# Optimization experiments

Measured on AMD Instinct MI355X. Metric: run time of the kernel, lower is better.

The kernel has to match this reference:

```python
import jax, jax.numpy as jnp
import numpy as np

B, C, T, V, P = 32, 64, 512, 54, 4
EPS = 1e-5


def setup_inputs() -> dict:
    key = jax.random.key(0)
    ks = jax.random.split(key, 5)
    x = jax.random.normal(ks[0], (B, C, T, V), dtype=jnp.float32)
    A = jax.random.uniform(ks[1], (P, V, V), dtype=jnp.float32)
    gweights = jax.random.normal(ks[2], (P, V, V), dtype=jnp.float32)
    W = jax.random.normal(ks[3], (P, C, C), dtype=jnp.float32) * 0.05  # (P, C_out, C_in)
    b = jax.random.normal(ks[4], (P, C), dtype=jnp.float32) * 0.05
    gamma = jnp.ones((C,), dtype=jnp.float32)
    beta = jnp.zeros((C,), dtype=jnp.float32)
    return {"x": x, "A": A, "gweights": gweights, "W": W, "b": b,
            "gamma": gamma, "beta": beta}


def reference(x, A, gweights, W, b, gamma, beta):
    # x: (B, C_in, T, V)
    Aeff = A * gweights  # (P, V, V), learned-weighted adjacency
    # per-part graph aggregation (x @ A_p) followed by 1x1 conv, summed over parts
    # out[b,o,t,v] = sum_p sum_c sum_u x[b,c,t,u] * Aeff[p,u,v] * W[p,o,c] + sum_p b[p,o]
    y = jnp.einsum('bctu,puv,poc->botv', x, Aeff, W, optimize=True)
    y = y + jnp.sum(b, axis=0)[None, :, None, None]
    # BatchNorm2d in training mode: batch stats over (B, T, V) per channel
    mean = jnp.mean(y, axis=(0, 2, 3), keepdims=True)
    var = jnp.mean(jnp.square(y - mean), axis=(0, 2, 3), keepdims=True)
    y = (y - mean) * jax.lax.rsqrt(var + EPS)
    y = y * gamma[None, :, None, None] + beta[None, :, None, None]
    y = jax.nn.relu(y)
    # temporal_conv is Identity (kernel_size=None); residual shortcut is Identity (C_in==C_out)
    return y + x
```

## Files before the change

### kernel.cpp

```cpp
#include <hip/hip_runtime.h>
#include <hip/hip_bf16.h>


typedef __bf16 bf16_t;
typedef __bf16 bf16x8 __attribute__((ext_vector_type(8)));
typedef __bf16 bf16x4 __attribute__((ext_vector_type(4)));
typedef float  f32x4  __attribute__((ext_vector_type(4)));
typedef unsigned int uint32;

static __device__ __forceinline__ f32x4 mfma16(bf16x8 a, bf16x8 b, f32x4 c) {
  return __builtin_amdgcn_mfma_f32_16x16x32_bf16(a, b, c, 0, 0, 0);
}
static __device__ __forceinline__ uint32 pk2(float a, float b) {
  union { __bf16 h; unsigned short u; } ua, ub;
  ua.h = (__bf16)a; ub.h = (__bf16)b;
  return (uint32)ua.u | ((uint32)ub.u << 16);
}

__global__ __launch_bounds__(256) void k_prep(
    const float* __restrict__ A, const float* __restrict__ g,
    const float* __restrict__ W, const float* __restrict__ bias,
    bf16_t* __restrict__ Wstk, bf16_t* __restrict__ At,
    float* __restrict__ bsum, float* __restrict__ stats) {
  int i = blockIdx.x * 256 + threadIdx.x;
  if (i < 16384) Wstk[i] = (bf16_t)W[i];
  if (i < 64 * 224) {
    int v = i / 224, pu = i - v * 224;
    float val = 0.f;
    if (v < 54 && pu < 216) { int idx = pu * 54 + v; val = A[idx] * g[idx]; }
    At[i] = (bf16_t)val;
  }
  if (i < 64) {
    float s = 0.f;
    for (int p = 0; p < 4; ++p) s += bias[p * 64 + i];
    bsum[i] = s;
  }
  if (i < 8192) stats[i] = 0.f;
}

__global__ __launch_bounds__(256) void k_tr(const float* __restrict__ x,
                                            bf16_t* __restrict__ xT) {
  __shared__ bf16_t T[256 * 66];
  const int tid = threadIdx.x;
  const int b = blockIdx.x / 108;
  const int rblk = blockIdx.x - b * 108;
  const int r0 = rblk << 8;
  const float* xb = x + (size_t)b * 64 * 27648 + r0;
  #pragma unroll 4
  for (int j = 0; j < 16; ++j) {
    int idx = tid + (j << 8);
    int c = idx >> 6, r4 = idx & 63;
    const float* src = xb + (size_t)c * 27648 + r4;
    #pragma unroll
    for (int k = 0; k < 4; ++k) {
      float v = src[k << 6];
      T[(r4 + (k << 6)) * 66 + c] = (bf16_t)v;
    }
  }
  __syncthreads();
  bf16_t* outb = xT + (((size_t)b * 27648 + r0) << 6);
  const uint32* Td = (const uint32*)T;
  #pragma unroll
  for (int j = 0; j < 8; ++j) {
    int row = (tid >> 3) + (j << 5);
    int seg = tid & 7;
    uint32 d0 = Td[row * 33 + (seg << 2) + 0];
    uint32 d1 = Td[row * 33 + (seg << 2) + 1];
    uint32 d2 = Td[row * 33 + (seg << 2) + 2];
    uint32 d3 = Td[row * 33 + (seg << 2) + 3];
    uint4 vv = make_uint4(d0, d1, d2, d3);
    *(uint4*)(outb + ((size_t)row << 6) + (seg << 3)) = vv;
  }
}

#define UPS 232

template<bool YBF16>
__global__ __launch_bounds__(256) void k_pass1(
    const bf16_t* __restrict__ xT, const bf16_t* __restrict__ Wstk,
    const bf16_t* __restrict__ At, const float* __restrict__ bsum,
    void* __restrict__ yprev, float* __restrict__ stats) {
  __shared__ bf16_t UpS[2][64 * UPS];

  const int tid  = threadIdx.x;
  const int bid  = blockIdx.x;
  const int b    = bid >> 7;
  const int t0   = (bid & 127) << 2;
  const int w    = tid >> 6;
  const int L    = tid & 63;
  const int quad = L >> 4;
  const int l15  = L & 15;

  for (int i = tid; i < 1024; i += 256) {
    int buf = i >> 9, row = (i >> 3) & 63, d = i & 7;
    ((uint32*)UpS[buf])[row * 116 + 108 + d] = 0u;
  }

  bf16x8 wb[4][2];
  #pragma unroll
  for (int ot = 0; ot < 4; ++ot)
    #pragma unroll
    for (int kk = 0; kk < 2; ++kk)
      wb[ot][kk] = *(const bf16x8*)(Wstk + (((w << 6) + (ot << 4) + l15) << 6)
                                          + (kk << 5) + (quad << 3));

  const int oc = (w << 4) + l15;
  const float bsv = bsum[oc];
  float ssum = 0.f, ssq = 0.f;

  for (int tt = 0; tt < 4; ++tt) {
    bf16_t* Up = UpS[tt & 1];
    const int t = t0 + tt;

    const bf16_t* xbase = xT + (((size_t)b * 27648 + (size_t)t * 54) << 6);
    bf16x8 xa[4][2];
    #pragma unroll
    for (int ut = 0; ut < 4; ++ut)
      #pragma unroll
      for (int kk = 0; kk < 2; ++kk)
        xa[ut][kk] = *(const bf16x8*)(xbase + (((ut << 4) + l15) << 6)
                                            + (kk << 5) + (quad << 3));
    #pragma unroll
    for (int ut = 0; ut < 4; ++ut) {
      const int u0 = (ut << 4) + (quad << 2);
      #pragma unroll
      for (int ot = 0; ot < 4; ++ot) {
        f32x4 acc = {0.f, 0.f, 0.f, 0.f};
        acc = mfma16(xa[ut][0], wb[ot][0], acc);
        acc = mfma16(xa[ut][1], wb[ot][1], acc);
        if (u0 < 54) {
          uint32* dst = (uint32*)(Up + ((ot << 4) + l15) * UPS + w * 54 + u0);
          dst[0] = pk2(acc[0], acc[1]);
          if (u0 + 3 < 54) dst[1] = pk2(acc[2], acc[3]);
        }
      }
    }
    __syncthreads();

    bf16x8 ub[7];
    #pragma unroll
    for (int kk = 0; kk < 7; ++kk)
      ub[kk] = *(const bf16x8*)(Up + ((w << 4) + l15) * UPS + (kk << 5) + (quad << 3));

    const size_t obase = (((size_t)((b << 6) + oc) << 9) + (size_t)t) * 54;
    #pragma unroll
    for (int mi = 0; mi < 4; ++mi) {
      f32x4 acc = {0.f, 0.f, 0.f, 0.f};
      #pragma unroll
      for (int kk = 0; kk < 7; ++kk) {
        bf16x8 av = *(const bf16x8*)(At + ((mi << 4) + l15) * 224
                                        + (kk << 5) + (quad << 3));
        acc = mfma16(av, ub[kk], acc);
      }
      const int v0 = (mi << 4) + (quad << 2);
      if (v0 + 3 < 54) {
        float y0 = acc[0] + bsv, y1 = acc[1] + bsv, y2 = acc[2] + bsv, y3 = acc[3] + bsv;
        if (YBF16) {
          uint32* d = (uint32*)((bf16_t*)yprev + obase + v0);
          d[0] = pk2(y0, y1); d[1] = pk2(y2, y3);
        } else {
          float2* d = (float2*)((float*)yprev + obase + v0);
          d[0] = make_float2(y0, y1); d[1] = make_float2(y2, y3);
        }
        ssum += y0 + y1 + y2 + y3;
        ssq  += y0 * y0 + y1 * y1 + y2 * y2 + y3 * y3;
      } else if (v0 == 52) {
        float y0 = acc[0] + bsv, y1 = acc[1] + bsv;
        if (YBF16) {
          *(uint32*)((bf16_t*)yprev + obase + v0) = pk2(y0, y1);
        } else {
          *(float2*)((float*)yprev + obase + v0) = make_float2(y0, y1);
        }
        ssum += y0 + y1;
        ssq  += y0 * y0 + y1 * y1;
      }
    }
    __syncthreads();
  }

  ssum += __shfl_xor(ssum, 16); ssq += __shfl_xor(ssq, 16);
  ssum += __shfl_xor(ssum, 32); ssq += __shfl_xor(ssq, 32);
  if (L < 16) {
    float* sb = stats + (bid & 63) * 128;
    atomicAdd(&sb[oc], ssum);
    atomicAdd(&sb[64 + oc], ssq);
  }
}

#define XT_STRIDE 72
#define UP_STRIDE 232
__global__ __launch_bounds__(256) void k_pass1_legacy(
    const float* __restrict__ x, const bf16_t* __restrict__ Wstk,
    const bf16_t* __restrict__ At, const float* __restrict__ bsum,
    float* __restrict__ ypre, float* __restrict__ stats) {
  __shared__ bf16_t XtS[4 * 54 * XT_STRIDE];
  __shared__ bf16_t UpS[64 * UP_STRIDE];
  const int tid = threadIdx.x, bid = blockIdx.x;
  const int b = bid >> 7, t0 = (bid & 127) << 2;
  const int w = tid >> 6, L = tid & 63, quad = L >> 4, l15 = L & 15;
  for (int i = tid; i < 64 * 8; i += 256)
    UpS[(i >> 3) * UP_STRIDE + 216 + (i & 7)] = (bf16_t)0.0f;
  const float* xb = x + (size_t)(b * 64 * 512 + t0) * 54;
  for (int j = tid; j < 64 * 216; j += 256) {
    int c = j / 216, r = j - c * 216;
    float v = xb[(size_t)c * 27648 + r];
    int tt = r / 54, u = r - tt * 54;
    XtS[(tt * 54 + u) * XT_STRIDE + c] = (bf16_t)v;
  }
  bf16x8 wfr[4][2];
  #pragma unroll
  for (int mi = 0; mi < 4; ++mi) {
    const bf16_t* arow = Wstk + (((((w << 2) + mi) << 4) + l15) * 64) + (quad << 3);
    #pragma unroll
    for (int kk = 0; kk < 2; ++kk) wfr[mi][kk] = *(const bf16x8*)(arow + kk * 32);
  }
  const int obase = (w << 4) + (quad << 2);
  float bs[4];
  #pragma unroll
  for (int r = 0; r < 4; ++r) bs[r] = bsum[obase + r];
  bf16x8 zf;
  #pragma unroll
  for (int j = 0; j < 8; ++j) zf[j] = (bf16_t)0.0f;
  float ssum[4] = {0.f,0.f,0.f,0.f}, ssq[4] = {0.f,0.f,0.f,0.f};
  __syncthreads();
  for (int tt = 0; tt < 4; ++tt) {
    bf16x8 xfr[4][2];
    #pragma unroll
    for (int nt = 0; nt < 4; ++nt) {
      const int urow = (nt << 4) + l15;
      #pragma unroll
      for (int kk = 0; kk < 2; ++kk) {
        xfr[nt][kk] = zf;
        if (urow < 54)
          xfr[nt][kk] = *(const bf16x8*)(&XtS[(tt * 54 + urow) * XT_STRIDE + kk * 32 + (quad << 3)]);
      }
    }
    #pragma unroll
    for (int mi = 0; mi < 4; ++mi) {
      f32x4 acc[4];
      #pragma unroll
      for (int nt = 0; nt < 4; ++nt)
        #pragma unroll
        for (int e = 0; e < 4; ++e) acc[nt][e] = 0.f;
      #pragma unroll
      for (int kk = 0; kk < 2; ++kk)
        #pragma unroll
        for (int nt = 0; nt < 4; ++nt)
          acc[nt] = mfma16(wfr[mi][kk], xfr[nt][kk], acc[nt]);
      #pragma unroll
      for (int nt = 0; nt < 4; ++nt) {
        const int u = (nt << 4) + l15;
        if (u < 54)
          #pragma unroll
          for (int r = 0; r < 4; ++r) {
            int o = (mi << 4) + (quad << 2) + r;
            UpS[o * UP_STRIDE + w * 54 + u] = (bf16_t)acc[nt][r];
          }
      }
    }
    __syncthreads();
    bf16x8 afr[7];
    #pragma unroll
    for (int kk = 0; kk < 7; ++kk)
      afr[kk] = *(const bf16x8*)(&UpS[((w << 4) + l15) * UP_STRIDE + kk * 32 + (quad << 3)]);
    f32x4 acc[4];
    #pragma unroll
    for (int nt = 0; nt < 4; ++nt)
      #pragma unroll
      for (int e = 0; e < 4; ++e) acc[nt][e] = 0.f;
    #pragma unroll
    for (int kk = 0; kk < 7; ++kk)
      #pragma unroll
      for (int nt = 0; nt < 4; ++nt) {
        bf16x8 bfr = *(const bf16x8*)(At + ((nt << 4) + l15) * 224 + kk * 32 + (quad << 3));
        acc[nt] = mfma16(afr[kk], bfr, acc[nt]);
      }
    const int t = t0 + tt;
    #pragma unroll
    for (int nt = 0; nt < 4; ++nt) {
      const int vcol = (nt << 4) + l15;
      if (vcol < 54)
        #pragma unroll
        for (int r = 0; r < 4; ++r) {
          float yv = acc[nt][r] + bs[r];
          ypre[(((size_t)b * 64 + (obase + r)) * 512 + t) * 54 + vcol] = yv;
          ssum[r] += yv; ssq[r] += yv * yv;
        }
    }
    __syncthreads();
  }
  #pragma unroll
  for (int off = 1; off < 16; off <<= 1)
    #pragma unroll
    for (int r = 0; r < 4; ++r) {
      ssum[r] += __shfl_xor(ssum[r], off);
      ssq[r]  += __shfl_xor(ssq[r], off);
    }
  if (l15 == 0) {
    float* sb = stats + (bid & 63) * 128;
    #pragma unroll
    for (int r = 0; r < 4; ++r) {
      atomicAdd(&sb[obase + r], ssum[r]);
      atomicAdd(&sb[64 + obase + r], ssq[r]);
    }
  }
}

__global__ void k_finalize(const float* __restrict__ gamma, const float* __restrict__ beta,
                           const float* __restrict__ stats, float* __restrict__ ac) {
  int o = threadIdx.x;
  if (o >= 64) return;
  float S = 0.f, Q = 0.f;
  for (int buf = 0; buf < 64; ++buf) {
    S += stats[buf * 128 + o];
    Q += stats[buf * 128 + 64 + o];
  }
  const float inv = 1.0f / 884736.0f;
  float mean = S * inv;
  float var  = Q * inv - mean * mean;
  float a = gamma[o] * rsqrtf(var + 1e-5f);
  ac[o] = a;
  ac[64 + o] = beta[o] - mean * a;
}

template<bool YBF16>
__global__ __launch_bounds__(256) void k_pass2(const float* __restrict__ x,
                                               const float* __restrict__ ac,
                                               const void* __restrict__ yprev,
                                               float* __restrict__ out) {
  const int slab = blockIdx.y;
  const int o = slab & 63;
  const size_t base = (size_t)slab * 27648 + (size_t)(((blockIdx.x << 8) + threadIdx.x) << 2);
  const float a = ac[o], c = ac[64 + o];
  float y0, y1, y2, y3;
  if (YBF16) {
    bf16x4 yp = *(const bf16x4*)((const bf16_t*)yprev + base);
    y0 = (float)yp[0]; y1 = (float)yp[1]; y2 = (float)yp[2]; y3 = (float)yp[3];
  } else {
    float4 yp = *(const float4*)((const float*)yprev + base);
    y0 = yp.x; y1 = yp.y; y2 = yp.z; y3 = yp.w;
  }
  float4 xv = *(const float4*)(x + base);
  float4 r;
  r.x = fmaxf(fmaf(a, y0, c), 0.f) + xv.x;
  r.y = fmaxf(fmaf(a, y1, c), 0.f) + xv.y;
  r.z = fmaxf(fmaf(a, y2, c), 0.f) + xv.z;
  r.w = fmaxf(fmaf(a, y3, c), 0.f) + xv.w;
  *(float4*)(out + base) = r;
}

extern "C" void kernel_launch(void* const* d_in, const int* in_sizes, int n_in,
                              void* d_out, int out_size, void* d_ws, size_t ws_size,
                              hipStream_t stream) {
  const float* x     = (const float*)d_in[0];
  const float* A     = (const float*)d_in[1];
  const float* g     = (const float*)d_in[2];
  const float* W     = (const float*)d_in[3];
  const float* bias  = (const float*)d_in[4];
  const float* gamma = (const float*)d_in[5];
  const float* beta  = (const float*)d_in[6];

  char* ws = (char*)d_ws;
  bf16_t* Wstk  = (bf16_t*)(ws + 0);
  bf16_t* At    = (bf16_t*)(ws + 32768);
  float*  bsum  = (float*)(ws + 61440);
  float*  stats = (float*)(ws + 61696);
  float*  ac    = (float*)(ws + 94464);
  const size_t XT_OFF   = 98304;
  const size_t XT_BYTES = (size_t)32 * 27648 * 64 * 2;
  const size_t YP_OFF   = XT_OFF + XT_BYTES;
  bf16_t* xT = (bf16_t*)(ws + XT_OFF);
  float*  out = (float*)d_out;

  const size_t need_primary = YP_OFF + XT_BYTES + 4096;
  const size_t need_fbA     = YP_OFF + 4096;

  k_prep<<<64, 256, 0, stream>>>(A, g, W, bias, Wstk, At, bsum, stats);

  if (ws_size >= need_primary) {
    bf16_t* ypre = (bf16_t*)(ws + YP_OFF);
    k_tr<<<3456, 256, 0, stream>>>(x, xT);
    k_pass1<true><<<4096, 256, 0, stream>>>(xT, Wstk, At, bsum, ypre, stats);
    k_finalize<<<1, 64, 0, stream>>>(gamma, beta, stats, ac);
    k_pass2<true><<<dim3(27, 2048), 256, 0, stream>>>(x, ac, ypre, out);
  } else if (ws_size >= need_fbA) {
    k_tr<<<3456, 256, 0, stream>>>(x, xT);
    k_pass1<false><<<4096, 256, 0, stream>>>(xT, Wstk, At, bsum, out, stats);
    k_finalize<<<1, 64, 0, stream>>>(gamma, beta, stats, ac);
    k_pass2<false><<<dim3(27, 2048), 256, 0, stream>>>(x, ac, out, out);
  } else {
    k_pass1_legacy<<<4096, 256, 0, stream>>>(x, Wstk, At, bsum, out, stats);
    k_finalize<<<1, 64, 0, stream>>>(gamma, beta, stats, ac);
    k_pass2<false><<<dim3(27, 2048), 256, 0, stream>>>(x, ac, out, out);
  }
}
```

Baseline: 610.5 us.

## Reorder einsum to apply adjacency first and drop transpose pass

Removes the separate x transpose kernel and its bf16 workspace copy. pass1 now reads fp32 x directly along the contiguous (t,v) axis, converts it to bf16 in registers, and multiplies by the adjacency first to form Z[v,(p,c)] in shared memory. A second MFMA stage contracts Z against a stacked W over K=256. It also prefetches the next timestep's x, uses a single shared buffer, and adds a launch-bounds occupancy hint. The first-stage loads are strided per lane, with a clamp to avoid reading past the end of x, and the contraction over u now includes padding work.

Measured after the change: 768.3 us. +25.8%, slower.

```diff
diff --git a/kernel.cpp b/kernel.cpp
--- a/kernel.cpp
+++ b/kernel.cpp
@@ -16,19 +16,52 @@
   ua.h = (__bf16)a; ub.h = (__bf16)b;
   return (uint32)ua.u | ((uint32)ub.u << 16);
 }
+static __device__ __forceinline__ bf16x8 cvt8(float2 a, float2 b, float2 c, float2 d) {
+  union { uint32 u[4]; bf16x8 v; } r;
+  r.u[0] = pk2(a.x, a.y); r.u[1] = pk2(b.x, b.y);
+  r.u[2] = pk2(c.x, c.y); r.u[3] = pk2(d.x, d.y);
+  return r.v;
+}
+
+#define XTOT 56623104ull
+
+static __device__ __forceinline__ void loadx(float2* pf, const float* __restrict__ x,
+                                             size_t xr) {
+  pf[0] = *(const float2*)(x + xr);
+  pf[1] = *(const float2*)(x + xr + 2);
+  pf[2] = *(const float2*)(x + xr + 4);
+  pf[3] = *(const float2*)(x + xr + 6);
+  const size_t LIM = XTOT - 2;
+  size_t o0 = xr + 32, o1 = xr + 34, o2 = xr + 36, o3 = xr + 38;
+  if (o0 > LIM) o0 = LIM;
+  if (o1 > LIM) o1 = LIM;
+  if (o2 > LIM) o2 = LIM;
+  if (o3 > LIM) o3 = LIM;
+  pf[4] = *(const float2*)(x + o0);
+  pf[5] = *(const float2*)(x + o1);
+  pf[6] = *(const float2*)(x + o2);
+  pf[7] = *(const float2*)(x + o3);
+}
 
 __global__ __launch_bounds__(256) void k_prep(
     const float* __restrict__ A, const float* __restrict__ g,
     const float* __restrict__ W, const float* __restrict__ bias,
-    bf16_t* __restrict__ Wstk, bf16_t* __restrict__ At,
+    bf16_t* __restrict__ W2, bf16_t* __restrict__ Ae,
     float* __restrict__ bsum, float* __restrict__ stats) {
   int i = blockIdx.x * 256 + threadIdx.x;
-  if (i < 16384) Wstk[i] = (bf16_t)W[i];
-  if (i < 64 * 224) {
-    int v = i / 224, pu = i - v * 224;
+  if (i < 16384) {
+    int o = i >> 8, k = i & 255, p = k >> 6, c = k & 63;
+    W2[i] = (bf16_t)W[p * 4096 + o * 64 + c];
+  }
+  if (i < 224 * 64) {
+    int pv = i >> 6, u = i & 63;
+    int p = pv / 56, v = pv - p * 56;
     float val = 0.f;
-    if (v < 54 && pu < 216) { int idx = pu * 54 + v; val = A[idx] * g[idx]; }
-    At[i] = (bf16_t)val;
+    if (v < 54 && u < 54) {
+      int idx = (p * 54 + u) * 54 + v;
+      val = A[idx] * g[idx];
+    }
+    Ae[i] = (bf16_t)val;
   }
   if (i < 64) {
     float s = 0.f;
@@ -38,49 +71,14 @@
   if (i < 8192) stats[i] = 0.f;
 }
 
-__global__ __launch_bounds__(256) void k_tr(const float* __restrict__ x,
-                                            bf16_t* __restrict__ xT) {
-  __shared__ bf16_t T[256 * 66];
-  const int tid = threadIdx.x;
-  const int b = blockIdx.x / 108;
-  const int rblk = blockIdx.x - b * 108;
-  const int r0 = rblk << 8;
-  const float* xb = x + (size_t)b * 64 * 27648 + r0;
-  #pragma unroll 4
-  for (int j = 0; j < 16; ++j) {
-    int idx = tid + (j << 8);
-    int c = idx >> 6, r4 = idx & 63;
-    const float* src = xb + (size_t)c * 27648 + r4;
-    #pragma unroll
-    for (int k = 0; k < 4; ++k) {
-      float v = src[k << 6];
-      T[(r4 + (k << 6)) * 66 + c] = (bf16_t)v;
-    }
-  }
-  __syncthreads();
-  bf16_t* outb = xT + (((size_t)b * 27648 + r0) << 6);
-  const uint32* Td = (const uint32*)T;
-  #pragma unroll
-  for (int j = 0; j < 8; ++j) {
-    int row = (tid >> 3) + (j << 5);
-    int seg = tid & 7;
-    uint32 d0 = Td[row * 33 + (seg << 2) + 0];
-    uint32 d1 = Td[row * 33 + (seg << 2) + 1];
-    uint32 d2 = Td[row * 33 + (seg << 2) + 2];
-    uint32 d3 = Td[row * 33 + (seg << 2) + 3];
-    uint4 vv = make_uint4(d0, d1, d2, d3);
-    *(uint4*)(outb + ((size_t)row << 6) + (seg << 3)) = vv;
-  }
-}
-
-#define UPS 232
+#define ZS 264
 
 template<bool YBF16>
-__global__ __launch_bounds__(256) void k_pass1(
-    const bf16_t* __restrict__ xT, const bf16_t* __restrict__ Wstk,
-    const bf16_t* __restrict__ At, const float* __restrict__ bsum,
+__global__ __launch_bounds__(256, 4) void k_pass1(
+    const float* __restrict__ x, const bf16_t* __restrict__ W2,
+    const bf16_t* __restrict__ Ae, const float* __restrict__ bsum,
     void* __restrict__ yprev, float* __restrict__ stats) {
-  __shared__ bf16_t UpS[2][64 * UPS];
+  __shared__ bf16_t Zt[64 * ZS];
 
   const int tid  = threadIdx.x;
   const int bid  = blockIdx.x;
@@ -91,66 +89,64 @@
   const int quad = L >> 4;
   const int l15  = L & 15;
 
-  for (int i = tid; i < 1024; i += 256) {
-    int buf = i >> 9, row = (i >> 3) & 63, d = i & 7;
-    ((uint32*)UpS[buf])[row * 116 + 108 + d] = 0u;
-  }
-
-  bf16x8 wb[4][2];
+  for (int i = tid; i < 8 * ZS / 2; i += 256)
+    ((uint32*)(Zt + 56 * ZS))[i] = 0u;
+
+  bf16x8 wf[8];
   #pragma unroll
-  for (int ot = 0; ot < 4; ++ot)
-    #pragma unroll
-    for (int kk = 0; kk < 2; ++kk)
-      wb[ot][kk] = *(const bf16x8*)(Wstk + (((w << 6) + (ot << 4) + l15) << 6)
-                                          + (kk << 5) + (quad << 3));
-
-  const int oc = (w << 4) + l15;
+  for (int kk = 0; kk < 8; ++kk)
+    wf[kk] = *(const bf16x8*)(W2 + (((w << 4) + l15) << 8) + (kk << 5) + (quad << 3));
+
+  int zoff[14];
+  #pragma unroll
+  for (int n = 0; n < 14; ++n) {
+    int pv = (n << 4) + l15;
+    int p = pv / 56;
+    int v = pv - p * 56;
+    zoff[n] = v * ZS + (p << 6) + (w << 4) + (quad << 2);
+  }
+
+  const int oc  = (w << 4) + l15;
   const float bsv = bsum[oc];
   float ssum = 0.f, ssq = 0.f;
 
+  const size_t xrow0 = (size_t)((b << 6) + oc) * 27648 + (quad << 3);
+
+  float2 pf[8];
+  loadx(pf, x, xrow0 + (size_t)t0 * 54);
+
   for (int tt = 0; tt < 4; ++tt) {
-    bf16_t* Up = UpS[tt & 1];
     const int t = t0 + tt;
 
-    const bf16_t* xbase = xT + (((size_t)b * 27648 + (size_t)t * 54) << 6);
-    bf16x8 xa[4][2];
+    bf16x8 xa0 = cvt8(pf[0], pf[1], pf[2], pf[3]);
+    bf16x8 xa1 = cvt8(pf[4], pf[5], pf[6], pf[7]);
+
+    __syncthreads();
+
     #pragma unroll
-    for (int ut = 0; ut < 4; ++ut)
-      #pragma unroll
-      for (int kk = 0; kk < 2; ++kk)
-        xa[ut][kk] = *(const bf16x8*)(xbase + (((ut << 4) + l15) << 6)
-                                            + (kk << 5) + (quad << 3));
-    #pragma unroll
-    for (int ut = 0; ut < 4; ++ut) {
-      const int u0 = (ut << 4) + (quad << 2);
-      #pragma unroll
-      for (int ot = 0; ot < 4; ++ot) {
-        f32x4 acc = {0.f, 0.f, 0.f, 0.f};
-        acc = mfma16(xa[ut][0], wb[ot][0], acc);
-        acc = mfma16(xa[ut][1], wb[ot][1], acc);
-        if (u0 < 54) {
-          uint32* dst = (uint32*)(Up + ((ot << 4) + l15) * UPS + w * 54 + u0);
-          dst[0] = pk2(acc[0], acc[1]);
-          if (u0 + 3 < 54) dst[1] = pk2(acc[2], acc[3]);
-        }
-      }
+    for (int n = 0; n < 14; ++n) {
+      const bf16_t* ar = Ae + (((n << 4) + l15) << 6) + (quad << 3);
+      f32x4 acc = {0.f, 0.f, 0.f, 0.f};
+      acc = mfma16(xa0, *(const bf16x8*)(ar), acc);
+      acc = mfma16(xa1, *(const bf16x8*)(ar + 32), acc);
+      uint32* dst = (uint32*)(Zt + zoff[n]);
+      dst[0] = pk2(acc[0], acc[1]);
+      dst[1] = pk2(acc[2], acc[3]);
     }
+
+    if (tt < 3) loadx(pf, x, xrow0 + (size_t)(t + 1) * 54);
+
     __syncthreads();
-
-    bf16x8 ub[7];
-    #pragma unroll
-    for (int kk = 0; kk < 7; ++kk)
-      ub[kk] = *(const bf16x8*)(Up + ((w << 4) + l15) * UPS + (kk << 5) + (quad << 3));
 
     const size_t obase = (((size_t)((b << 6) + oc) << 9) + (size_t)t) * 54;
     #pragma unroll
     for (int mi = 0; mi < 4; ++mi) {
       f32x4 acc = {0.f, 0.f, 0.f, 0.f};
       #pragma unroll
-      for (int kk = 0; kk < 7; ++kk) {
-        bf16x8 av = *(const bf16x8*)(At + ((mi << 4) + l15) * 224
+      for (int kk = 0; kk < 8; ++kk) {
+        bf16x8 za = *(const bf16x8*)(Zt + ((mi << 4) + l15) * ZS
                                         + (kk << 5) + (quad << 3));
-        acc = mfma16(av, ub[kk], acc);
+        acc = mfma16(za, wf[kk], acc);
       }
       const int v0 = (mi << 4) + (quad << 2);
       if (v0 + 3 < 54) {
@@ -175,7 +171,6 @@
         ssq  += y0 * y0 + y1 * y1;
       }
     }
-    __syncthreads();
   }
 
   ssum += __shfl_xor(ssum, 16); ssq += __shfl_xor(ssq, 16);
@@ -184,125 +179,6 @@
     float* sb = stats + (bid & 63) * 128;
     atomicAdd(&sb[oc], ssum);
     atomicAdd(&sb[64 + oc], ssq);
-  }
-}
-
-#define XT_STRIDE 72
-#define UP_STRIDE 232
-__global__ __launch_bounds__(256) void k_pass1_legacy(
-    const float* __restrict__ x, const bf16_t* __restrict__ Wstk,
-    const bf16_t* __restrict__ At, const float* __restrict__ bsum,
-    float* __restrict__ ypre, float* __restrict__ stats) {
-  __shared__ bf16_t XtS[4 * 54 * XT_STRIDE];
-  __shared__ bf16_t UpS[64 * UP_STRIDE];
-  const int tid = threadIdx.x, bid = blockIdx.x;
-  const int b = bid >> 7, t0 = (bid & 127) << 2;
-  const int w = tid >> 6, L = tid & 63, quad = L >> 4, l15 = L & 15;
-  for (int i = tid; i < 64 * 8; i += 256)
-    UpS[(i >> 3) * UP_STRIDE + 216 + (i & 7)] = (bf16_t)0.0f;
-  const float* xb = x + (size_t)(b * 64 * 512 + t0) * 54;
-  for (int j = tid; j < 64 * 216; j += 256) {
-    int c = j / 216, r = j - c * 216;
-    float v = xb[(size_t)c * 27648 + r];
-    int tt = r / 54, u = r - tt * 54;
-    XtS[(tt * 54 + u) * XT_STRIDE + c] = (bf16_t)v;
-  }
-  bf16x8 wfr[4][2];
-  #pragma unroll
-  for (int mi = 0; mi < 4; ++mi) {
-    const bf16_t* arow = Wstk + (((((w << 2) + mi) << 4) + l15) * 64) + (quad << 3);
-    #pragma unroll
-    for (int kk = 0; kk < 2; ++kk) wfr[mi][kk] = *(const bf16x8*)(arow + kk * 32);
-  }
-  const int obase = (w << 4) + (quad << 2);
-  float bs[4];
-  #pragma unroll
-  for (int r = 0; r < 4; ++r) bs[r] = bsum[obase + r];
-  bf16x8 zf;
-  #pragma unroll
-  for (int j = 0; j < 8; ++j) zf[j] = (bf16_t)0.0f;
-  float ssum[4] = {0.f,0.f,0.f,0.f}, ssq[4] = {0.f,0.f,0.f,0.f};
-  __syncthreads();
-  for (int tt = 0; tt < 4; ++tt) {
-    bf16x8 xfr[4][2];
-    #pragma unroll
-    for (int nt = 0; nt < 4; ++nt) {
-      const int urow = (nt << 4) + l15;
-      #pragma unroll
-      for (int kk = 0; kk < 2; ++kk) {
-        xfr[nt][kk] = zf;
-        if (urow < 54)
-          xfr[nt][kk] = *(const bf16x8*)(&XtS[(tt * 54 + urow) * XT_STRIDE + kk * 32 + (quad << 3)]);
-      }
-    }
-    #pragma unroll
-    for (int mi = 0; mi < 4; ++mi) {
-      f32x4 acc[4];
-      #pragma unroll
-      for (int nt = 0; nt < 4; ++nt)
-        #pragma unroll
-        for (int e = 0; e < 4; ++e) acc[nt][e] = 0.f;
-      #pragma unroll
-      for (int kk = 0; kk < 2; ++kk)
-        #pragma unroll
-        for (int nt = 0; nt < 4; ++nt)
-          acc[nt] = mfma16(wfr[mi][kk], xfr[nt][kk], acc[nt]);
-      #pragma unroll
-      for (int nt = 0; nt < 4; ++nt) {
-        const int u = (nt << 4) + l15;
-        if (u < 54)
-          #pragma unroll
-          for (int r = 0; r < 4; ++r) {
-            int o = (mi << 4) + (quad << 2) + r;
-            UpS[o * UP_STRIDE + w * 54 + u] = (bf16_t)acc[nt][r];
-          }
-      }
-    }
-    __syncthreads();
-    bf16x8 afr[7];
-    #pragma unroll
-    for (int kk = 0; kk < 7; ++kk)
-      afr[kk] = *(const bf16x8*)(&UpS[((w << 4) + l15) * UP_STRIDE + kk * 32 + (quad << 3)]);
-    f32x4 acc[4];
-    #pragma unroll
-    for (int nt = 0; nt < 4; ++nt)
-      #pragma unroll
-      for (int e = 0; e < 4; ++e) acc[nt][e] = 0.f;
-    #pragma unroll
-    for (int kk = 0; kk < 7; ++kk)
-      #pragma unroll
-      for (int nt = 0; nt < 4; ++nt) {
-        bf16x8 bfr = *(const bf16x8*)(At + ((nt << 4) + l15) * 224 + kk * 32 + (quad << 3));
-        acc[nt] = mfma16(afr[kk], bfr, acc[nt]);
-      }
-    const int t = t0 + tt;
-    #pragma unroll
-    for (int nt = 0; nt < 4; ++nt) {
-      const int vcol = (nt << 4) + l15;
-      if (vcol < 54)
-        #pragma unroll
-        for (int r = 0; r < 4; ++r) {
-          float yv = acc[nt][r] + bs[r];
-          ypre[(((size_t)b * 64 + (obase + r)) * 512 + t) * 54 + vcol] = yv;
-          ssum[r] += yv; ssq[r] += yv * yv;
-        }
-    }
-    __syncthreads();
-  }
-  #pragma unroll
-  for (int off = 1; off < 16; off <<= 1)
-    #pragma unroll
-    for (int r = 0; r < 4; ++r) {
-      ssum[r] += __shfl_xor(ssum[r], off);
-      ssq[r]  += __shfl_xor(ssq[r], off);
-    }
-  if (l15 == 0) {
-    float* sb = stats + (bid & 63) * 128;
-    #pragma unroll
-    for (int r = 0; r < 4; ++r) {
-      atomicAdd(&sb[obase + r], ssum[r]);
-      atomicAdd(&sb[64 + obase + r], ssq[r]);
-    }
   }
 }
 
@@ -361,36 +237,25 @@
   const float* beta  = (const float*)d_in[6];
 
   char* ws = (char*)d_ws;
-  bf16_t* Wstk  = (bf16_t*)(ws + 0);
-  bf16_t* At    = (bf16_t*)(ws + 32768);
+  bf16_t* W2    = (bf16_t*)(ws + 0);
+  bf16_t* Ae    = (bf16_t*)(ws + 32768);
   float*  bsum  = (float*)(ws + 61440);
   float*  stats = (float*)(ws + 61696);
   float*  ac    = (float*)(ws + 94464);
-  const size_t XT_OFF   = 98304;
-  const size_t XT_BYTES = (size_t)32 * 27648 * 64 * 2;
-  const size_t YP_OFF   = XT_OFF + XT_BYTES;
-  bf16_t* xT = (bf16_t*)(ws + XT_OFF);
-  float*  out = (float*)d_out;
-
-  const size_t need_primary = YP_OFF + XT_BYTES + 4096;
-  const size_t need_fbA     = YP_OFF + 4096;
-
-  k_prep<<<64, 256, 0, stream>>>(A, g, W, bias, Wstk, At, bsum, stats);
-
-  if (ws_size >= need_primary) {
+  const size_t YP_OFF   = 98304;
+  const size_t YP_BYTES = (size_t)32 * 64 * 512 * 54 * 2;
+  float* out = (float*)d_out;
+
+  k_prep<<<64, 256, 0, stream>>>(A, g, W, bias, W2, Ae, bsum, stats);
+
+  if (ws_size >= YP_OFF + YP_BYTES + 4096) {
     bf16_t* ypre = (bf16_t*)(ws + YP_OFF);
-    k_tr<<<3456, 256, 0, stream>>>(x, xT);
-    k_pass1<true><<<4096, 256, 0, stream>>>(xT, Wstk, At, bsum, ypre, stats);
+    k_pass1<true><<<4096, 256, 0, stream>>>(x, W2, Ae, bsum, ypre, stats);
     k_finalize<<<1, 64, 0, stream>>>(gamma, beta, stats, ac);
     k_pass2<true><<<dim3(27, 2048), 256, 0, stream>>>(x, ac, ypre, out);
-  } else if (ws_size >= need_fbA) {
-    k_tr<<<3456, 256, 0, stream>>>(x, xT);
-    k_pass1<false><<<4096, 256, 0, stream>>>(xT, Wstk, At, bsum, out, stats);
+  } else {
+    k_pass1<false><<<4096, 256, 0, stream>>>(x, W2, Ae, bsum, out, stats);
     k_finalize<<<1, 64, 0, stream>>>(gamma, beta, stats, ac);
     k_pass2<false><<<dim3(27, 2048), 256, 0, stream>>>(x, ac, out, out);
-  } else {
-    k_pass1_legacy<<<4096, 256, 0, stream>>>(x, Wstk, At, bsum, out, stats);
-    k_finalize<<<1, 64, 0, stream>>>(gamma, beta, stats, ac);
-    k_pass2<false><<<dim3(27, 2048), 256, 0, stream>>>(x, ac, out, out);
-  }
-}
+  }
+}
```
